# Optimization experiments

Hardware: AMD Instinct MI355X
Metric: run time of the kernel (lower is better)

The kernel has to match this reference:

```python
import jax, jax.numpy as jnp
import numpy as np

N, M, P = 32, 16, 32
B, T = 256, 200
STD_DYN, STD_OBS = 0.1, 0.1


def setup_inputs() -> dict:
    key = jax.random.key(0)
    k = jax.random.split(key, 6)
    Y = jax.random.normal(k[0], (B, T, P), dtype=jnp.float32)
    U = jax.random.normal(k[1], (B, T, M), dtype=jnp.float32)
    mask = jnp.ones((B, T), dtype=jnp.float32)
    # stable transition matrix
    A = 0.95 * jnp.eye(N, dtype=jnp.float32) + 0.05 * jax.random.normal(k[2], (N, N), dtype=jnp.float32) / np.sqrt(N)
    Bm = jax.random.normal(k[3], (N, M), dtype=jnp.float32) / np.sqrt(M)
    C = jax.random.normal(k[4], (P, N), dtype=jnp.float32) / np.sqrt(N)
    mu0 = jax.random.normal(k[5], (N,), dtype=jnp.float32)
    Sigma0 = jnp.eye(N, dtype=jnp.float32)
    Q = (STD_DYN ** 2) * jnp.eye(N, dtype=jnp.float32)
    R = (STD_OBS ** 2) * jnp.eye(P, dtype=jnp.float32)
    return {"Y": Y, "U": U, "mask": mask, "A": A, "Bm": Bm, "C": C,
            "mu0": mu0, "Sigma0": Sigma0, "Q": Q, "R": R}


def _sym(X):
    return 0.5 * (X + jnp.swapaxes(X, -1, -2))


def reference(Y, U, mask, A, Bm, C, mu0, Sigma0, Q, R):
    """Kalman filter forward pass (time-invariant A,B,C; Q,R diag buffers).
    Returns (mus_filt [B,T,n], Sigmas_filt [B,T,n,n], mus_pred [B,T,n],
             Sigmas_pred [B,T,n,n])."""
    Bsz = Y.shape[0]
    n = A.shape[0]
    I = jnp.eye(n, dtype=Y.dtype)

    mu_init = jnp.broadcast_to(mu0, (Bsz, n))                 # [B,n]
    Sig_init = jnp.broadcast_to(Sigma0, (Bsz, n, n))          # [B,n,n]

    def step(carry, inp):
        mu, Sigma = carry                                     # [B,n], [B,n,n]
        y_t, u_t, m_t = inp                                   # [B,p], [B,m], [B]
        # predict
        mu_pred = mu @ A.T + u_t @ Bm.T                       # [B,n]
        Sigma_pred = jnp.einsum('ij,bjk,lk->bil', A, Sigma, A) + Q
        # innovation
        r = y_t - mu_pred @ C.T                               # [B,p]
        S = _sym(jnp.einsum('ij,bjk,lk->bil', C, Sigma_pred, C) + R)  # [B,p,p]
        PCT = jnp.einsum('bij,kj->bik', Sigma_pred, C)        # [B,n,p]
        # gain: K = (solve(S, PCT^T))^T
        K = jnp.swapaxes(jnp.linalg.solve(S, jnp.swapaxes(PCT, -1, -2)), -1, -2)
        K = m_t[:, None, None] * K                            # mask missing obs
        # update (Joseph form)
        mu_new = mu_pred + jnp.einsum('bnp,bp->bn', K, r)
        I_KC = I - K @ C                                      # [B,n,n]
        Sigma_new = _sym(jnp.einsum('bij,bjk,blk->bil', I_KC, Sigma_pred, I_KC)
                         + jnp.einsum('bip,pq,bjq->bij', K, R, K))
        return (mu_new, Sigma_new), (mu_new, Sigma_new, mu_pred, Sigma_pred)

    xs = (jnp.swapaxes(Y, 0, 1), jnp.swapaxes(U, 0, 1), jnp.swapaxes(mask, 0, 1))
    _, (mf, Sf, mp, Sp) = jax.lax.scan(step, (mu_init, Sig_init), xs)
    # [T,B,...] -> [B,T,...]
    return (jnp.swapaxes(mf, 0, 1), jnp.swapaxes(Sf, 0, 1),
            jnp.swapaxes(mp, 0, 1), jnp.swapaxes(Sp, 0, 1))
```

## Files before the change

### kernel.cpp

```cpp
#include <hip/hip_runtime.h>
#include <math.h>

#define TT 200
#define ST 36
#define PA 33

__device__ __forceinline__ float rdlane(float v, int l) {
  return __int_as_float(__builtin_amdgcn_readlane(__float_as_int(v), l));
}

#if __has_builtin(__builtin_amdgcn_rsqf)
#define RSQF(x) __builtin_amdgcn_rsqf(x)
#else
#define RSQF(x) (1.0f / sqrtf(x))
#endif

__device__ __forceinline__ float4 ld4(const float* p) { return *(const float4*)p; }
__device__ __forceinline__ void st4(float* p, float4 v) { *(float4*)p = v; }

__device__ __forceinline__ float dot32r(const float* __restrict__ row, const float (&a)[32]) {
  float s0 = 0.f, s1 = 0.f;
  #pragma unroll
  for (int k = 0; k < 32; k += 8) {
    float4 v0 = ld4(row + k);
    float4 v1 = ld4(row + k + 4);
    s0 = fmaf(a[k+0], v0.x, s0); s0 = fmaf(a[k+1], v0.y, s0);
    s0 = fmaf(a[k+2], v0.z, s0); s0 = fmaf(a[k+3], v0.w, s0);
    s1 = fmaf(a[k+4], v1.x, s1); s1 = fmaf(a[k+5], v1.y, s1);
    s1 = fmaf(a[k+6], v1.z, s1); s1 = fmaf(a[k+7], v1.w, s1);
  }
  return s0 + s1;
}

__device__ __forceinline__ float dot32rr(const float* __restrict__ ra, const float* __restrict__ rb) {
  float s0 = 0.f, s1 = 0.f;
  #pragma unroll
  for (int k = 0; k < 32; k += 8) {
    float4 x0 = ld4(ra + k), x1 = ld4(ra + k + 4);
    float4 y0 = ld4(rb + k), y1 = ld4(rb + k + 4);
    s0 = fmaf(x0.x, y0.x, s0); s0 = fmaf(x0.y, y0.y, s0);
    s0 = fmaf(x0.z, y0.z, s0); s0 = fmaf(x0.w, y0.w, s0);
    s1 = fmaf(x1.x, y1.x, s1); s1 = fmaf(x1.y, y1.y, s1);
    s1 = fmaf(x1.z, y1.z, s1); s1 = fmaf(x1.w, y1.w, s1);
  }
  return s0 + s1;
}

__global__ void __launch_bounds__(512, 2) kf_kernel(
    const float* __restrict__ Yg, const float* __restrict__ Ug,
    const float* __restrict__ Mg, const float* __restrict__ Ag,
    const float* __restrict__ Bg, const float* __restrict__ Cg,
    const float* __restrict__ mu0g, const float* __restrict__ S0g,
    const float* __restrict__ Qg, const float* __restrict__ Rg,
    float* __restrict__ out, int Bsz)
{
  __shared__ __align__(16) float SIG[32*ST];
  __shared__ __align__(16) float T1[32*ST];
  __shared__ __align__(16) float SIGP[32*ST];
  __shared__ __align__(16) float T2R[32*ST];
  __shared__ __align__(16) float SR[32*ST];
  __shared__ __align__(16) float WT[33*ST];
  __shared__ __align__(16) float QL[1024], RL[1024];
  __shared__ float ALDS[32*PA], CLDS[32*PA];
  __shared__ float u_lds[16], y_lds[32], mupred[32], mu_lds[32], mlds[2];

  const int tid = threadIdx.x;
  const int mi = tid >> 4;
  const int c  = tid & 15;
  const int b = blockIdx.x;
  const long btB = (long)b * TT;

  const long o_Sf = (long)Bsz * TT * 32;
  const long o_mp = o_Sf + (long)Bsz * TT * 32 * 32;
  const long o_Sp = o_mp + (long)Bsz * TT * 32;

  for (int e = tid; e < 1024; e += 512) {
    int i = e >> 5, k = e & 31;
    ALDS[i*PA + k] = Ag[e];
    CLDS[i*PA + k] = Cg[e];
    QL[e] = Qg[e];
    RL[e] = Rg[e];
    SIG[i*ST + k] = S0g[e];
  }
  if (tid < 32) mu_lds[tid] = mu0g[tid];
  if (tid < 16) u_lds[tid] = Ug[btB*16 + tid];
  if (tid >= 64 && tid < 96) y_lds[tid-64] = Yg[btB*32 + (tid-64)];
  if (tid == 224) mlds[0] = Mg[btB];

  float a_row[32], c_row[32];
  #pragma unroll
  for (int k = 0; k < 32; k += 4) {
    float4 va = ld4(Ag + mi*32 + k);
    a_row[k] = va.x; a_row[k+1] = va.y; a_row[k+2] = va.z; a_row[k+3] = va.w;
    float4 vc = ld4(Cg + mi*32 + k);
    c_row[k] = vc.x; c_row[k+1] = vc.y; c_row[k+2] = vc.z; c_row[k+3] = vc.w;
  }
  __syncthreads();

  for (int t = 0; t < TT; ++t) {
    const long bt = btB + t;

    {
      float t1a = dot32r(SIG + c*ST, a_row);
      float t1b = dot32r(SIG + (c+16)*ST, a_row);
      T1[mi*ST + c]      = t1a;
      T1[mi*ST + c + 16] = t1b;
    }
    __syncthreads();

    {
      float va = dot32r(T1 + c*ST, a_row)      + QL[mi*32 + c];
      float vb = dot32r(T1 + (c+16)*ST, a_row) + QL[mi*32 + c + 16];
      SIGP[mi*ST + c]      = va;
      SIGP[mi*ST + c + 16] = vb;
      if (tid < 32) {
        float s = 0.f;
        #pragma unroll
        for (int k = 0; k < 32; ++k) s = fmaf(ALDS[tid*PA + k], mu_lds[k], s);
        #pragma unroll
        for (int k = 0; k < 16; ++k) s = fmaf(Bg[tid*16 + k], u_lds[k], s);
        mupred[tid] = s;
      }
    }
    __syncthreads();

    {
      float ta = dot32r(SIGP + c*ST, c_row);
      float tb = dot32r(SIGP + (c+16)*ST, c_row);
      T2R[mi*ST + c]      = ta;
      T2R[mi*ST + c + 16] = tb;
      if (tid < 32) {
        float s = y_lds[tid];
        #pragma unroll
        for (int k = 0; k < 32; ++k) s = fmaf(-CLDS[tid*PA + k], mupred[k], s);
        T2R[tid*ST + 32] = s;
      }
    }
    __syncthreads();

    {
      float sa = dot32r(T2R + c*ST, c_row)      + RL[mi*32 + c];
      float sb = dot32r(T2R + (c+16)*ST, c_row) + RL[mi*32 + c + 16];
      SR[mi*ST + c]      = sa;
      SR[mi*ST + c + 16] = sb;
    }
    __syncthreads();

    if (tid < 64) {
      int cc = tid; if (cc > 32) cc = 32;
      float w[32], rr[32];
      #pragma unroll
      for (int i = 0; i < 32; ++i) {
        w[i]  = 0.5f * (SR[i*ST + cc] + SR[cc*ST + i]);
        rr[i] = T2R[i*ST + cc];
      }
      #pragma unroll
      for (int j = 0; j < 32; ++j) {
        float d  = rdlane(w[j], j);
        float s  = RSQF(d);
        float cj = w[j] * s;
        float zj = rr[j] * s;
        rr[j] = zj;
        WT[cc*ST + j] = zj;
        float scj = s * cj;
        #pragma unroll
        for (int i = j+1; i < 32; ++i) {
          float bw = rdlane(w[i], j);
          w[i]  = fmaf(-bw, scj, w[i]);
          rr[i] = fmaf(-(bw * s), zj, rr[i]);
        }
      }
    } else {
      const int u = tid - 64;
      if (u < 256) {
        st4(out + o_Sp + bt*1024 + u*4, ld4(SIGP + (u>>3)*ST + (u&7)*4));
      } else if (t > 0) {
        const int q = u - 256;
        st4(out + o_Sf + (bt-1)*1024 + q*4, ld4(SIG + (q>>3)*ST + (q&7)*4));
      }
      if (u < 64 && t > 0) {
        const int q = u + 192;
        st4(out + o_Sf + (bt-1)*1024 + q*4, ld4(SIG + (q>>3)*ST + (q&7)*4));
      }
      if (tid >= 64 && tid < 96)  out[o_mp + bt*32 + (tid-64)] = mupred[tid-64];
      if (t > 0 && tid >= 96 && tid < 128) out[(bt-1)*32 + (tid-96)] = mu_lds[tid-96];
      if (t < TT-1) {
        if (tid >= 128 && tid < 144) u_lds[tid-128] = Ug[(bt+1)*16 + (tid-128)];
        if (tid >= 160 && tid < 192) y_lds[tid-160] = Yg[(bt+1)*32 + (tid-160)];
        if (tid == 200) mlds[(t+1)&1] = Mg[bt+1];
      }
    }
    __syncthreads();

    {
      const float m = mlds[t&1];
      const float coefS = fmaf(m, m, -2.f*m);
      float wm[32];
      #pragma unroll
      for (int k = 0; k < 32; k += 4) {
        float4 v = ld4(WT + mi*ST + k);
        wm[k] = v.x; wm[k+1] = v.y; wm[k+2] = v.z; wm[k+3] = v.w;
      }
      float ga = dot32r(WT + c*ST, wm);
      float gb = dot32r(WT + (c+16)*ST, wm);
      float spa = SIGP[mi*ST + c];
      float spb = SIGP[mi*ST + c + 16];
      SIG[mi*ST + c]      = fmaf(coefS, ga, spa);
      SIG[mi*ST + c + 16] = fmaf(coefS, gb, spb);
      if (tid < 32) {
        float sacc = dot32rr(WT + tid*ST, WT + 32*ST);
        mu_lds[tid] = fmaf(m, sacc, mupred[tid]);
      }
    }
    __syncthreads();
  }

  {
    const long bt = btB + TT - 1;
    if (tid < 256)
      st4(out + o_Sf + bt*1024 + tid*4, ld4(SIG + (tid>>3)*ST + (tid&7)*4));
    if (tid >= 480)
      out[bt*32 + (tid - 480)] = mu_lds[tid - 480];
  }
}

extern "C" void kernel_launch(void* const* d_in, const int* in_sizes, int n_in,
                              void* d_out, int out_size, void* d_ws, size_t ws_size,
                              hipStream_t stream) {
  const float* Y   = (const float*)d_in[0];
  const float* U   = (const float*)d_in[1];
  const float* Mk  = (const float*)d_in[2];
  const float* A   = (const float*)d_in[3];
  const float* Bm  = (const float*)d_in[4];
  const float* C   = (const float*)d_in[5];
  const float* mu0 = (const float*)d_in[6];
  const float* S0  = (const float*)d_in[7];
  const float* Q   = (const float*)d_in[8];
  const float* R   = (const float*)d_in[9];
  int Bsz = in_sizes[2] / TT;
  kf_kernel<<<Bsz, 512, 0, stream>>>(Y, U, Mk, A, Bm, C, mu0, S0, Q, R,
                                     (float*)d_out, Bsz);
}
```

Measured before the change: 1.971 ms.

## Remap matmul threads so each reads one LDS row against two register rows

Threads are remapped from (row mi, two columns c/c+16) to (column r, two output rows q/q+16). Each thread now holds two A rows and two C rows in registers, so each LDS row load feeds two dot products and LDS reads per output drop by half. The Cholesky step stops symmetrizing S on read and uses a reformulated update with fewer multiplies. The cost is doubled register arrays (128 floats), which may pressure occupancy under launch_bounds(512,2), and changed LDS write patterns with possible bank conflicts.

```diff
diff --git a/kernel.cpp b/kernel.cpp
--- a/kernel.cpp
+++ b/kernel.cpp
@@ -30,6 +30,26 @@
     s1 = fmaf(a[k+6], v1.z, s1); s1 = fmaf(a[k+7], v1.w, s1);
   }
   return s0 + s1;
+}
+
+__device__ __forceinline__ void dot32x2(const float* __restrict__ row,
+                                        const float (&a)[32], const float (&b)[32],
+                                        float& oa, float& ob) {
+  float a0=0.f, a1=0.f, b0=0.f, b1=0.f;
+  #pragma unroll
+  for (int k = 0; k < 32; k += 8) {
+    float4 v0 = ld4(row + k);
+    float4 v1 = ld4(row + k + 4);
+    a0 = fmaf(a[k+0], v0.x, a0); a1 = fmaf(a[k+1], v0.y, a1);
+    a0 = fmaf(a[k+2], v0.z, a0); a1 = fmaf(a[k+3], v0.w, a1);
+    b0 = fmaf(b[k+0], v0.x, b0); b1 = fmaf(b[k+1], v0.y, b1);
+    b0 = fmaf(b[k+2], v0.z, b0); b1 = fmaf(b[k+3], v0.w, b1);
+    a0 = fmaf(a[k+4], v1.x, a0); a1 = fmaf(a[k+5], v1.y, a1);
+    a0 = fmaf(a[k+6], v1.z, a0); a1 = fmaf(a[k+7], v1.w, a1);
+    b0 = fmaf(b[k+4], v1.x, b0); b1 = fmaf(b[k+5], v1.y, b1);
+    b0 = fmaf(b[k+6], v1.z, b0); b1 = fmaf(b[k+7], v1.w, b1);
+  }
+  oa = a0 + a1; ob = b0 + b1;
 }
 
 __device__ __forceinline__ float dot32rr(const float* __restrict__ ra, const float* __restrict__ rb) {
@@ -65,8 +85,8 @@
   __shared__ float u_lds[16], y_lds[32], mupred[32], mu_lds[32], mlds[2];
 
   const int tid = threadIdx.x;
-  const int mi = tid >> 4;
-  const int c  = tid & 15;
+  const int q = tid >> 5;
+  const int r = tid & 31;
   const int b = blockIdx.x;
   const long btB = (long)b * TT;
 
@@ -87,32 +107,27 @@
   if (tid >= 64 && tid < 96) y_lds[tid-64] = Yg[btB*32 + (tid-64)];
   if (tid == 224) mlds[0] = Mg[btB];
 
-  float a_row[32], c_row[32];
+  float aq0[32], aq1[32], cq0[32], cq1[32];
   #pragma unroll
   for (int k = 0; k < 32; k += 4) {
-    float4 va = ld4(Ag + mi*32 + k);
-    a_row[k] = va.x; a_row[k+1] = va.y; a_row[k+2] = va.z; a_row[k+3] = va.w;
-    float4 vc = ld4(Cg + mi*32 + k);
-    c_row[k] = vc.x; c_row[k+1] = vc.y; c_row[k+2] = vc.z; c_row[k+3] = vc.w;
+    float4 v;
+    v = ld4(Ag + q*32 + k);        aq0[k]=v.x; aq0[k+1]=v.y; aq0[k+2]=v.z; aq0[k+3]=v.w;
+    v = ld4(Ag + (q+16)*32 + k);   aq1[k]=v.x; aq1[k+1]=v.y; aq1[k+2]=v.z; aq1[k+3]=v.w;
+    v = ld4(Cg + q*32 + k);        cq0[k]=v.x; cq0[k+1]=v.y; cq0[k+2]=v.z; cq0[k+3]=v.w;
+    v = ld4(Cg + (q+16)*32 + k);   cq1[k]=v.x; cq1[k+1]=v.y; cq1[k+2]=v.z; cq1[k+3]=v.w;
   }
   __syncthreads();
+
+  const int ro0 = q*ST + r;
+  const int ro1 = (q+16)*ST + r;
 
   for (int t = 0; t < TT; ++t) {
     const long bt = btB + t;
 
     {
-      float t1a = dot32r(SIG + c*ST, a_row);
-      float t1b = dot32r(SIG + (c+16)*ST, a_row);
-      T1[mi*ST + c]      = t1a;
-      T1[mi*ST + c + 16] = t1b;
-    }
-    __syncthreads();
-
-    {
-      float va = dot32r(T1 + c*ST, a_row)      + QL[mi*32 + c];
-      float vb = dot32r(T1 + (c+16)*ST, a_row) + QL[mi*32 + c + 16];
-      SIGP[mi*ST + c]      = va;
-      SIGP[mi*ST + c + 16] = vb;
+      float ta, tb;
+      dot32x2(SIG + r*ST, aq0, aq1, ta, tb);
+      T1[ro0] = ta; T1[ro1] = tb;
       if (tid < 32) {
         float s = 0.f;
         #pragma unroll
@@ -125,10 +140,10 @@
     __syncthreads();
 
     {
-      float ta = dot32r(SIGP + c*ST, c_row);
-      float tb = dot32r(SIGP + (c+16)*ST, c_row);
-      T2R[mi*ST + c]      = ta;
-      T2R[mi*ST + c + 16] = tb;
+      float va, vb;
+      dot32x2(T1 + r*ST, aq0, aq1, va, vb);
+      SIGP[ro0] = va + QL[q*32 + r];
+      SIGP[ro1] = vb + QL[(q+16)*32 + r];
       if (tid < 32) {
         float s = y_lds[tid];
         #pragma unroll
@@ -139,10 +154,17 @@
     __syncthreads();
 
     {
-      float sa = dot32r(T2R + c*ST, c_row)      + RL[mi*32 + c];
-      float sb = dot32r(T2R + (c+16)*ST, c_row) + RL[mi*32 + c + 16];
-      SR[mi*ST + c]      = sa;
-      SR[mi*ST + c + 16] = sb;
+      float ta, tb;
+      dot32x2(SIGP + r*ST, cq0, cq1, ta, tb);
+      T2R[ro0] = ta; T2R[ro1] = tb;
+    }
+    __syncthreads();
+
+    {
+      float sa, sb;
+      dot32x2(T2R + r*ST, cq0, cq1, sa, sb);
+      SR[ro0] = sa + RL[q*32 + r];
+      SR[ro1] = sb + RL[(q+16)*32 + r];
     }
     __syncthreads();
 
@@ -151,23 +173,22 @@
       float w[32], rr[32];
       #pragma unroll
       for (int i = 0; i < 32; ++i) {
-        w[i]  = 0.5f * (SR[i*ST + cc] + SR[cc*ST + i]);
+        w[i]  = SR[i*ST + cc];
         rr[i] = T2R[i*ST + cc];
       }
       #pragma unroll
       for (int j = 0; j < 32; ++j) {
         float d  = rdlane(w[j], j);
-        float s  = RSQF(d);
-        float cj = w[j] * s;
-        float zj = rr[j] * s;
-        rr[j] = zj;
-        WT[cc*ST + j] = zj;
-        float scj = s * cj;
+        float sj = RSQF(d);
+        float s2 = sj * sj;
+        float gw = s2 * w[j];
+        float gr = s2 * rr[j];
+        WT[cc*ST + j] = rr[j] * sj;
         #pragma unroll
         for (int i = j+1; i < 32; ++i) {
           float bw = rdlane(w[i], j);
-          w[i]  = fmaf(-bw, scj, w[i]);
-          rr[i] = fmaf(-(bw * s), zj, rr[i]);
+          w[i]  = fmaf(-bw, gw, w[i]);
+          rr[i] = fmaf(-bw, gr, rr[i]);
         }
       }
     } else {
@@ -175,12 +196,12 @@
       if (u < 256) {
         st4(out + o_Sp + bt*1024 + u*4, ld4(SIGP + (u>>3)*ST + (u&7)*4));
       } else if (t > 0) {
-        const int q = u - 256;
-        st4(out + o_Sf + (bt-1)*1024 + q*4, ld4(SIG + (q>>3)*ST + (q&7)*4));
+        const int q2 = u - 256;
+        st4(out + o_Sf + (bt-1)*1024 + q2*4, ld4(SIG + (q2>>3)*ST + (q2&7)*4));
       }
       if (u < 64 && t > 0) {
-        const int q = u + 192;
-        st4(out + o_Sf + (bt-1)*1024 + q*4, ld4(SIG + (q>>3)*ST + (q&7)*4));
+        const int q2 = u + 192;
+        st4(out + o_Sf + (bt-1)*1024 + q2*4, ld4(SIG + (q2>>3)*ST + (q2&7)*4));
       }
       if (tid >= 64 && tid < 96)  out[o_mp + bt*32 + (tid-64)] = mupred[tid-64];
       if (t > 0 && tid >= 96 && tid < 128) out[(bt-1)*32 + (tid-96)] = mu_lds[tid-96];
@@ -195,18 +216,16 @@
     {
       const float m = mlds[t&1];
       const float coefS = fmaf(m, m, -2.f*m);
-      float wm[32];
+      float rv[32];
       #pragma unroll
       for (int k = 0; k < 32; k += 4) {
-        float4 v = ld4(WT + mi*ST + k);
-        wm[k] = v.x; wm[k+1] = v.y; wm[k+2] = v.z; wm[k+3] = v.w;
-      }
-      float ga = dot32r(WT + c*ST, wm);
-      float gb = dot32r(WT + (c+16)*ST, wm);
-      float spa = SIGP[mi*ST + c];
-      float spb = SIGP[mi*ST + c + 16];
-      SIG[mi*ST + c]      = fmaf(coefS, ga, spa);
-      SIG[mi*ST + c + 16] = fmaf(coefS, gb, spb);
+        float4 v = ld4(WT + r*ST + k);
+        rv[k] = v.x; rv[k+1] = v.y; rv[k+2] = v.z; rv[k+3] = v.w;
+      }
+      float ga = dot32r(WT + q*ST, rv);
+      float gb = dot32r(WT + (q+16)*ST, rv);
+      SIG[ro0] = fmaf(coefS, ga, SIGP[ro0]);
+      SIG[ro1] = fmaf(coefS, gb, SIGP[ro1]);
       if (tid < 32) {
         float sacc = dot32rr(WT + tid*ST, WT + 32*ST);
         mu_lds[tid] = fmaf(m, sacc, mupred[tid]);
```

New measurement: 1.653 ms. -16.2%, faster.
